# Performance work log

Measured on AMD Instinct MI355X. Metric: run time of the kernel, lower is better.

The kernel has to match this reference:

```python
import jax, jax.numpy as jnp
import numpy as np

D_IN = 512
D_OUT = 512


def setup_inputs() -> dict:
    key = jax.random.key(0)
    ks = jax.random.split(key, 7)
    B, S = 4, 4096
    sc = 1.0 / np.sqrt(D_IN)
    return {
        "x": jax.random.normal(ks[0], (B, S, D_IN), dtype=jnp.float32),
        "Wq": jax.random.normal(ks[1], (D_IN, D_OUT), dtype=jnp.float32) * sc,
        "bq": jnp.zeros((D_OUT,), dtype=jnp.float32),
        "Wk": jax.random.normal(ks[2], (D_IN, D_OUT), dtype=jnp.float32) * sc,
        "bk": jnp.zeros((D_OUT,), dtype=jnp.float32),
        "Wv": jax.random.normal(ks[3], (D_IN, D_OUT), dtype=jnp.float32) * sc,
        "bv": jnp.zeros((D_OUT,), dtype=jnp.float32),
    }


def reference(x, Wq, bq, Wk, bk, Wv, bv):
    # Linear projections
    Q = x @ Wq + bq  # [B,S,Do]
    K = x @ Wk + bk
    V = x @ Wv + bv
    # NOTE: original torch code computes `len(K) ** 1 / 2` which is
    # (len(K)**1)/2 = batch_size / 2 due to operator precedence (not sqrt).
    scale = x.shape[0] / 2.0
    scores = jnp.einsum("bsd,btd->bst", Q, K) / scale  # [B,S,S]
    a = jax.nn.softmax(scores, axis=-1)
    Z = jnp.einsum("bst,btd->bsd", a, V)  # [B,S,Do]
    return Z
```

## Files before the change

### kernel.cpp

```cpp
#include <hip/hip_runtime.h>

typedef _Float16 h8 __attribute__((ext_vector_type(8)));
typedef float f4 __attribute__((ext_vector_type(4)));

#define MFMA16(a, b, c) __builtin_amdgcn_mfma_f32_16x16x32_f16((a), (b), (c), 0, 0, 0)

__device__ static inline void gl_lds16(const void* g, void* l) {
  __builtin_amdgcn_global_load_lds((const __attribute__((address_space(1))) unsigned int*)g,
                                   (__attribute__((address_space(3))) unsigned int*)l, 16, 0, 0);
}

__device__ static inline unsigned encf(float f) {
  unsigned u = __float_as_uint(f);
  return (u & 0x80000000u) ? ~u : (u | 0x80000000u);
}
__device__ static inline float decf(unsigned u) {
  return __uint_as_float((u & 0x80000000u) ? (u ^ 0x80000000u) : ~u);
}


__global__ void wconv_kernel(const float* __restrict__ Wq, const float* __restrict__ Wk,
                             const float* __restrict__ Wv, _Float16* __restrict__ Wt,
                             unsigned* __restrict__ mEnc) {
  int idx = blockIdx.x * 256 + threadIdx.x;
  if (idx < 16384) mEnc[idx] = 0u;
  int z = idx >> 15, rem = idx & 32767;
  int n = rem >> 6, k0 = (rem & 63) << 3;
  const float* W = (z == 0) ? Wq : (z == 1) ? Wk : Wv;
  float sc = (z == 0) ? 0.5f : 1.0f;
  h8 v;
#pragma unroll
  for (int j = 0; j < 8; ++j) v[j] = (_Float16)(W[(k0 + j) * 512 + n] * sc);
  size_t blk = (size_t)((z * 4 + (n >> 7)) * 8 + (k0 >> 6));
  int off = (n & 127) * 64 + ((((k0 >> 3) & 7) ^ (n & 7)) << 3);
  *(h8*)&Wt[blk * 8192 + off] = v;
}

__global__ __launch_bounds__(256, 3)
void proj_kernel(const float* __restrict__ x, const _Float16* __restrict__ Wt,
                 const float* __restrict__ bq, const float* __restrict__ bk,
                 const float* __restrict__ bv,
                 char* __restrict__ Qimg, char* __restrict__ Kimg, char* __restrict__ VTimg) {
  __shared__ _Float16 sMem[16384];
  _Float16* sA = sMem;
  _Float16* sB = sMem + 8192;
  const int tid = threadIdx.x;
  const int wave = tid >> 6, lane = tid & 63;
  const int quad = lane >> 4, lr = lane & 15;
  const int mbase = blockIdx.x * 128, nbase = blockIdx.y * 128, z = blockIdx.z;
  const int sr = tid >> 1, sseg = tid & 1;
  const int rbase = (wave & 1) * 64, cbase = (wave >> 1) * 64;
  const char* WtB = (const char*)Wt + ((size_t)(z * 4 + (nbase >> 7)) * 8) * 16384;

  float4 ax[8];
  f4 acc[4][4];
#pragma unroll
  for (int i = 0; i < 4; ++i)
#pragma unroll
    for (int j = 0; j < 4; ++j) { f4 zz = {0.f, 0.f, 0.f, 0.f}; acc[i][j] = zz; }

  {
    const float4* asrc = (const float4*)&x[(size_t)(mbase + sr) * 512 + sseg * 32];
#pragma unroll
    for (int i = 0; i < 8; ++i) ax[i] = asrc[i];
#pragma unroll
    for (int j = 0; j < 4; ++j)
      gl_lds16(WtB + tid * 16 + j * 4096, (char*)sB + tid * 16 + j * 4096);
  }

  for (int kt = 0; kt < 8; ++kt) {
    if (kt > 0) __syncthreads();
#pragma unroll
    for (int i = 0; i < 4; ++i) {
      h8 v;
      float4 f0 = ax[2 * i], f1 = ax[2 * i + 1];
      v[0] = (_Float16)f0.x; v[1] = (_Float16)f0.y; v[2] = (_Float16)f0.z; v[3] = (_Float16)f0.w;
      v[4] = (_Float16)f1.x; v[5] = (_Float16)f1.y; v[6] = (_Float16)f1.z; v[7] = (_Float16)f1.w;
      *(h8*)&sA[sr * 64 + (((sseg * 4 + i) ^ (sr & 7)) << 3)] = v;
    }
    if (kt > 0) {
#pragma unroll
      for (int j = 0; j < 4; ++j)
        gl_lds16(WtB + kt * 16384 + tid * 16 + j * 4096, (char*)sB + tid * 16 + j * 4096);
    }
    __syncthreads();
    if (kt < 7) {
      const float4* asrc = (const float4*)&x[(size_t)(mbase + sr) * 512 + (kt + 1) * 64 + sseg * 32];
#pragma unroll
      for (int i = 0; i < 8; ++i) ax[i] = asrc[i];
    }
#pragma unroll
    for (int ks = 0; ks < 2; ++ks) {
      h8 a[4], bb[4];
#pragma unroll
      for (int rt = 0; rt < 4; ++rt) {
        const int r = rbase + rt * 16 + lr;
        a[rt] = *(const h8*)&sA[r * 64 + ((((ks << 2) | quad) ^ (lr & 7)) << 3)];
      }
#pragma unroll
      for (int ct = 0; ct < 4; ++ct) {
        const int r = cbase + ct * 16 + lr;
        bb[ct] = *(const h8*)&sB[r * 64 + ((((ks << 2) | quad) ^ (lr & 7)) << 3)];
      }
#pragma unroll
      for (int rt = 0; rt < 4; ++rt)
#pragma unroll
        for (int ct = 0; ct < 4; ++ct)
          acc[rt][ct] = MFMA16(a[rt], bb[ct], acc[rt][ct]);
    }
  }

  const float* bias = (z == 0) ? bq : (z == 1) ? bk : bv;
  const float bscale = (z == 0) ? 0.5f : 1.0f;
  _Float16* sC = sMem;
  __syncthreads();
#pragma unroll
  for (int ct = 0; ct < 4; ++ct) {
    const int dl = cbase + ct * 16 + lr;
    const float bb = bias[nbase + dl] * bscale;
#pragma unroll
    for (int rt = 0; rt < 4; ++rt) {
#pragma unroll
      for (int r = 0; r < 4; ++r) {
        const int sl = rbase + rt * 16 + quad * 4 + r;
        const _Float16 val = (_Float16)(acc[rt][ct][r] + bb);
        if (z == 2) {
          sC[((sl >> 6) << 13) + dl * 64 + ((((sl >> 3) & 7) ^ (dl & 7)) << 3) + (sl & 7)] = val;
        } else {
          sC[((dl >> 6) << 13) + sl * 64 + ((((dl >> 3) & 7) ^ (sl & 7)) << 3) + (dl & 7)] = val;
        }
      }
    }
  }
  __syncthreads();
  const int b_ = mbase >> 12;
  char* dst;
  if (z != 2) {
    char* img = (z == 0) ? Qimg : Kimg;
    dst = img + ((size_t)((b_ * 32 + ((mbase & 4095) >> 7)) * 8 + (nbase >> 6) + (tid >> 7))) * 16384;
  } else {
    dst = VTimg + ((size_t)((b_ * 4 + (nbase >> 7)) * 64 + ((mbase & 4095) >> 6) + (tid >> 7))) * 16384;
  }
  dst += (size_t)(tid & 127) * 128;
#pragma unroll
  for (int k = 0; k < 8; ++k)
    *(int4*)(dst + k * 16) = *(const int4*)&sC[tid * 64 + k * 8];
}

__global__ __launch_bounds__(256, 3)
void qk_kernel(const char* __restrict__ Qimg, const char* __restrict__ Kimg,
               char* __restrict__ S, unsigned* __restrict__ mEnc, int b0, int s0) {
  __shared__ _Float16 sMem[16384];
  _Float16* sA = sMem;
  _Float16* sB = sMem + 8192;
  const int tid = threadIdx.x;
  const int wave = tid >> 6, lane = tid & 63;
  const int quad = lane >> 4, lr = lane & 15;
  const int cb = blockIdx.x;
  const int rbL = blockIdx.z * gridDim.y + blockIdx.y;
  const int b = b0 + blockIdx.z;
  const int rbase = (wave & 1) * 64, cbase = (wave >> 1) * 64;
  const char* Ab = Qimg + ((size_t)((b * 32 + (s0 >> 7) + blockIdx.y) * 8)) * 16384;
  const char* Bb = Kimg + ((size_t)((b * 32 + cb) * 8)) * 16384;

  f4 acc[4][4];
#pragma unroll
  for (int i = 0; i < 4; ++i)
#pragma unroll
    for (int j = 0; j < 4; ++j) { f4 zz = {0.f, 0.f, 0.f, 0.f}; acc[i][j] = zz; }

#pragma unroll
  for (int j = 0; j < 4; ++j) {
    gl_lds16(Ab + tid * 16 + j * 4096, (char*)sA + tid * 16 + j * 4096);
    gl_lds16(Bb + tid * 16 + j * 4096, (char*)sB + tid * 16 + j * 4096);
  }

  for (int kt = 0; kt < 8; ++kt) {
    asm volatile("s_waitcnt vmcnt(0)" ::: "memory");
    __builtin_amdgcn_s_barrier();
    __builtin_amdgcn_sched_barrier(0);
    h8 a[4][2], bb[4][2];
#pragma unroll
    for (int ks = 0; ks < 2; ++ks) {
#pragma unroll
      for (int rt = 0; rt < 4; ++rt) {
        const int r = rbase + rt * 16 + lr;
        a[rt][ks] = *(const h8*)&sA[r * 64 + ((((ks << 2) | quad) ^ (lr & 7)) << 3)];
      }
#pragma unroll
      for (int ct = 0; ct < 4; ++ct) {
        const int r = cbase + ct * 16 + lr;
        bb[ct][ks] = *(const h8*)&sB[r * 64 + ((((ks << 2) | quad) ^ (lr & 7)) << 3)];
      }
    }
    asm volatile("s_waitcnt lgkmcnt(0)" ::: "memory");
    __builtin_amdgcn_s_barrier();
    __builtin_amdgcn_sched_barrier(0);
    if (kt < 7) {
#pragma unroll
      for (int j = 0; j < 4; ++j) {
        gl_lds16(Ab + (kt + 1) * 16384 + tid * 16 + j * 4096, (char*)sA + tid * 16 + j * 4096);
        gl_lds16(Bb + (kt + 1) * 16384 + tid * 16 + j * 4096, (char*)sB + tid * 16 + j * 4096);
      }
    }
    __builtin_amdgcn_s_setprio(1);
#pragma unroll
    for (int ks = 0; ks < 2; ++ks)
#pragma unroll
      for (int rt = 0; rt < 4; ++rt)
#pragma unroll
        for (int ct = 0; ct < 4; ++ct)
          acc[rt][ct] = MFMA16(a[rt][ks], bb[ct][ks], acc[rt][ct]);
    __builtin_amdgcn_s_setprio(0);
  }

  {
    const int growb = b * 4096 + s0 + blockIdx.y * 128;
#pragma unroll
    for (int rt = 0; rt < 4; ++rt) {
#pragma unroll
      for (int r = 0; r < 4; ++r) {
        float mx = fmaxf(fmaxf(acc[rt][0][r], acc[rt][1][r]),
                         fmaxf(acc[rt][2][r], acc[rt][3][r]));
        mx = fmaxf(mx, __shfl_xor(mx, 1));
        mx = fmaxf(mx, __shfl_xor(mx, 2));
        mx = fmaxf(mx, __shfl_xor(mx, 4));
        mx = fmaxf(mx, __shfl_xor(mx, 8));
        if (lr == 0)
          atomicMax(&mEnc[growb + rbase + rt * 16 + quad * 4 + r], encf(mx));
      }
    }
  }

  _Float16* sC = sMem;
  __syncthreads();
#pragma unroll
  for (int ct = 0; ct < 4; ++ct) {
    const int tl = cbase + ct * 16 + lr;
#pragma unroll
    for (int rt = 0; rt < 4; ++rt) {
#pragma unroll
      for (int r = 0; r < 4; ++r) {
        const int sl = rbase + rt * 16 + quad * 4 + r;
        sC[((tl >> 6) << 13) + sl * 64 + ((((tl >> 3) & 7) ^ (sl & 7)) << 3) + (tl & 7)] =
            (_Float16)acc[rt][ct][r];
      }
    }
  }
  __syncthreads();
  char* dst = S + ((size_t)(rbL * 64 + cb * 2 + (tid >> 7))) * 16384 + (size_t)(tid & 127) * 128;
#pragma unroll
  for (int k = 0; k < 8; ++k)
    *(int4*)(dst + k * 16) = *(const int4*)&sC[tid * 64 + k * 8];
}

__global__ __launch_bounds__(256, 4)
void pv_kernel(const char* __restrict__ S, const char* __restrict__ VTimg,
               const unsigned* __restrict__ mEnc, float* __restrict__ out, int b0, int s0) {
  __shared__ _Float16 sMem[12288];
  __shared__ float ls[64];
  _Float16* sA = sMem;
  _Float16* sB = sMem + 4096;
  const int tid = threadIdx.x;
  const int wave = tid >> 6, lane = tid & 63;
  const int quad = lane >> 4, lr = lane & 15;
  const int db = blockIdx.x;
  const int sbL = blockIdx.z * gridDim.y + blockIdx.y;
  const int b = b0 + blockIdx.z;
  const int rbase = (wave & 1) * 32, cbase = (wave >> 1) * 64;
  const char* Ab = S + ((size_t)((sbL >> 1) * 64)) * 16384 + (size_t)(sbL & 1) * 8192;
  const char* Bb = VTimg + ((size_t)((b * 4 + db) * 64)) * 16384;

  const int lrow = tid >> 3;
  const int growb = b * 4096 + s0 + blockIdx.y * 64;
  const float m0 = decf(mEnc[growb + lrow]);
  const float m1 = decf(mEnc[growb + 32 + lrow]);
  float rs0 = 0.f, rs1 = 0.f;

  f4 acc[2][4];
#pragma unroll
  for (int i = 0; i < 2; ++i)
#pragma unroll
    for (int j = 0; j < 4; ++j) { f4 zz = {0.f, 0.f, 0.f, 0.f}; acc[i][j] = zz; }

  {
#pragma unroll
    for (int j = 0; j < 4; ++j)
      gl_lds16(Bb + tid * 16 + j * 4096, (char*)sB + tid * 16 + j * 4096);
    {
      h8 ha = *(const h8*)(Ab + tid * 16);
      h8 w;
#pragma unroll
      for (int u = 0; u < 8; ++u) { float e = __expf((float)ha[u] - m0); w[u] = (_Float16)e; rs0 += e; }
      *(h8*)((char*)sA + tid * 16) = w;
    }
    {
      h8 ha = *(const h8*)(Ab + tid * 16 + 4096);
      h8 w;
#pragma unroll
      for (int u = 0; u < 8; ++u) { float e = __expf((float)ha[u] - m1); w[u] = (_Float16)e; rs1 += e; }
      *(h8*)((char*)sA + tid * 16 + 4096) = w;
    }
  }

  for (int kt = 0; kt < 64; ++kt) {
    asm volatile("s_waitcnt vmcnt(0) lgkmcnt(0)" ::: "memory");
    __builtin_amdgcn_s_barrier();
    __builtin_amdgcn_sched_barrier(0);
    h8 a[2][2], bb[4][2];
#pragma unroll
    for (int ks = 0; ks < 2; ++ks) {
#pragma unroll
      for (int rt = 0; rt < 2; ++rt) {
        const int r = rbase + rt * 16 + lr;
        a[rt][ks] = *(const h8*)&sA[r * 64 + ((((ks << 2) | quad) ^ (lr & 7)) << 3)];
      }
#pragma unroll
      for (int ct = 0; ct < 4; ++ct) {
        const int r = cbase + ct * 16 + lr;
        bb[ct][ks] = *(const h8*)&sB[r * 64 + ((((ks << 2) | quad) ^ (lr & 7)) << 3)];
      }
    }
    h8 ha0, ha1;
    if (kt < 63) {
      ha0 = *(const h8*)(Ab + (kt + 1) * 16384 + tid * 16);
      ha1 = *(const h8*)(Ab + (kt + 1) * 16384 + tid * 16 + 4096);
    }
    asm volatile("s_waitcnt lgkmcnt(0)" ::: "memory");
    __builtin_amdgcn_s_barrier();
    __builtin_amdgcn_sched_barrier(0);
    if (kt < 63) {
#pragma unroll
      for (int j = 0; j < 4; ++j)
        gl_lds16(Bb + (kt + 1) * 16384 + tid * 16 + j * 4096, (char*)sB + tid * 16 + j * 4096);
      h8 w0, w1;
#pragma unroll
      for (int u = 0; u < 8; ++u) { float e = __expf((float)ha0[u] - m0); w0[u] = (_Float16)e; rs0 += e; }
#pragma unroll
      for (int u = 0; u < 8; ++u) { float e = __expf((float)ha1[u] - m1); w1[u] = (_Float16)e; rs1 += e; }
      *(h8*)((char*)sA + tid * 16) = w0;
      *(h8*)((char*)sA + tid * 16 + 4096) = w1;
    }
    __builtin_amdgcn_s_setprio(1);
#pragma unroll
    for (int ks = 0; ks < 2; ++ks)
#pragma unroll
      for (int rt = 0; rt < 2; ++rt)
#pragma unroll
        for (int ct = 0; ct < 4; ++ct)
          acc[rt][ct] = MFMA16(a[rt][ks], bb[ct][ks], acc[rt][ct]);
    __builtin_amdgcn_s_setprio(0);
  }

  rs0 += __shfl_xor(rs0, 1); rs0 += __shfl_xor(rs0, 2); rs0 += __shfl_xor(rs0, 4);
  rs1 += __shfl_xor(rs1, 1); rs1 += __shfl_xor(rs1, 2); rs1 += __shfl_xor(rs1, 4);
  if ((tid & 7) == 0) { ls[lrow] = rs0; ls[32 + lrow] = rs1; }
  __syncthreads();

#pragma unroll
  for (int rt = 0; rt < 2; ++rt) {
#pragma unroll
    for (int r = 0; r < 4; ++r) {
      const int lrw = rbase + rt * 16 + quad * 4 + r;
      const int srow = s0 + blockIdx.y * 64 + lrw;
      const float li = 1.0f / ls[lrw];
      float* op = &out[((size_t)b * 4096 + srow) * 512 + db * 128];
#pragma unroll
      for (int ct = 0; ct < 4; ++ct)
        op[cbase + ct * 16 + lr] = acc[rt][ct][r] * li;
    }
  }
}

extern "C" void kernel_launch(void* const* d_in, const int* in_sizes, int n_in,
                              void* d_out, int out_size, void* d_ws, size_t ws_size,
                              hipStream_t stream) {
  (void)in_sizes; (void)n_in; (void)out_size;
  const float* x  = (const float*)d_in[0];
  const float* Wq = (const float*)d_in[1];
  const float* bq = (const float*)d_in[2];
  const float* Wk = (const float*)d_in[3];
  const float* bk = (const float*)d_in[4];
  const float* Wv = (const float*)d_in[5];
  const float* bv = (const float*)d_in[6];
  float* out = (float*)d_out;
  char* ws = (char*)d_ws;
  char* Qimg  = ws;
  char* Kimg  = ws + ((size_t)16 << 20);
  char* VTimg = ws + ((size_t)32 << 20);
  _Float16* Wt = (_Float16*)(ws + ((size_t)48 << 20));
  unsigned* mEnc = (unsigned*)(ws + ((size_t)50 << 20) - 65536);
  char* Simg   = ws + ((size_t)50 << 20);

  wconv_kernel<<<dim3(384), dim3(256), 0, stream>>>(Wq, Wk, Wv, Wt, mEnc);
  proj_kernel<<<dim3(128, 4, 3), dim3(256), 0, stream>>>(x, Wt, bq, bk, bv, Qimg, Kimg, VTimg);

  const size_t avail = ws_size > ((size_t)50 << 20) ? ws_size - ((size_t)50 << 20) : 0;
  int nchunk, nb, Ms;
  if      (avail >= ((size_t)128 << 20)) { nchunk = 1;  nb = 4; Ms = 4096; }
  else if (avail >= ((size_t)64  << 20)) { nchunk = 2;  nb = 2; Ms = 4096; }
  else if (avail >= ((size_t)32  << 20)) { nchunk = 4;  nb = 1; Ms = 4096; }
  else if (avail >= ((size_t)16  << 20)) { nchunk = 8;  nb = 1; Ms = 2048; }
  else if (avail >= ((size_t)8   << 20)) { nchunk = 16; nb = 1; Ms = 1024; }
  else                                   { nchunk = 32; nb = 1; Ms = 512;  }
  const int chunksPerBatch = 4096 / Ms;

  for (int c = 0; c < nchunk; ++c) {
    int b0, s0;
    if (nb > 1 || Ms == 4096) { b0 = c * nb; s0 = 0; }
    else { b0 = c / chunksPerBatch; s0 = (c % chunksPerBatch) * Ms; }
    qk_kernel<<<dim3(32, Ms / 128, nb), dim3(256), 0, stream>>>(Qimg, Kimg, Simg, mEnc, b0, s0);
    pv_kernel<<<dim3(4, Ms / 64, nb), dim3(256), 0, stream>>>(Simg, VTimg, mEnc, out, b0, s0);
  }
}
```

Before: 405.1 us.

## Widen PV kernel to full 512-column tiles with double-buffered LDS pipeline

The PV kernel now uses 512-thread blocks where each block computes all 512 output columns for 64 rows. Previously four blocks each took a 128-column slice and each recomputed exp over the same S tile. The S tile and the V^T tiles are double-buffered in about 144KB of LDS, so the next tile's global loads overlap the current MFMAs. This leaves one barrier per K step instead of two, and a swizzled block index spreads batches across CUs. The aims are to remove the fourfold redundant exp and S reads and to hide load latency. The cost is one block per CU from the large LDS footprint, more accumulator registers, and a grid four times smaller.

```diff
diff --git a/kernel.cpp b/kernel.cpp
--- a/kernel.cpp
+++ b/kernel.cpp
@@ -254,107 +254,119 @@
     *(int4*)(dst + k * 16) = *(const int4*)&sC[tid * 64 + k * 8];
 }
 
-__global__ __launch_bounds__(256, 4)
+__global__ __launch_bounds__(512, 2)
 void pv_kernel(const char* __restrict__ S, const char* __restrict__ VTimg,
-               const unsigned* __restrict__ mEnc, float* __restrict__ out, int b0, int s0) {
-  __shared__ _Float16 sMem[12288];
+               const unsigned* __restrict__ mEnc, float* __restrict__ out,
+               int b0, int s0, int nyb, int nb) {
+  __shared__ _Float16 sMem[73728];
   __shared__ float ls[64];
-  _Float16* sA = sMem;
-  _Float16* sB = sMem + 4096;
   const int tid = threadIdx.x;
   const int wave = tid >> 6, lane = tid & 63;
   const int quad = lane >> 4, lr = lane & 15;
-  const int db = blockIdx.x;
-  const int sbL = blockIdx.z * gridDim.y + blockIdx.y;
-  const int b = b0 + blockIdx.z;
-  const int rbase = (wave & 1) * 32, cbase = (wave >> 1) * 64;
+  const int flat = blockIdx.x;
+  int bL, yl;
+  if (nb == 4) { bL = (flat & 7) >> 1; yl = ((flat >> 3) << 1) | (flat & 1); }
+  else { bL = flat / nyb; yl = flat - bL * nyb; }
+  const int b = b0 + bL;
+  const int sbL = bL * nyb + yl;
+  const int rbase = (wave & 1) * 32, cbase = (wave >> 1) * 128;
   const char* Ab = S + ((size_t)((sbL >> 1) * 64)) * 16384 + (size_t)(sbL & 1) * 8192;
-  const char* Bb = VTimg + ((size_t)((b * 4 + db) * 64)) * 16384;
+  const char* Bb = VTimg + ((size_t)(b * 4) * 64) * 16384;
 
   const int lrow = tid >> 3;
-  const int growb = b * 4096 + s0 + blockIdx.y * 64;
+  const int growb = b * 4096 + s0 + yl * 64;
   const float m0 = decf(mEnc[growb + lrow]);
-  const float m1 = decf(mEnc[growb + 32 + lrow]);
-  float rs0 = 0.f, rs1 = 0.f;
-
-  f4 acc[2][4];
+  float rs = 0.f;
+
+  f4 acc[2][8];
 #pragma unroll
   for (int i = 0; i < 2; ++i)
 #pragma unroll
-    for (int j = 0; j < 4; ++j) { f4 zz = {0.f, 0.f, 0.f, 0.f}; acc[i][j] = zz; }
+    for (int j = 0; j < 8; ++j) { f4 zz = {0.f, 0.f, 0.f, 0.f}; acc[i][j] = zz; }
 
   {
-#pragma unroll
-    for (int j = 0; j < 4; ++j)
-      gl_lds16(Bb + tid * 16 + j * 4096, (char*)sB + tid * 16 + j * 4096);
-    {
-      h8 ha = *(const h8*)(Ab + tid * 16);
-      h8 w;
-#pragma unroll
-      for (int u = 0; u < 8; ++u) { float e = __expf((float)ha[u] - m0); w[u] = (_Float16)e; rs0 += e; }
-      *(h8*)((char*)sA + tid * 16) = w;
-    }
-    {
-      h8 ha = *(const h8*)(Ab + tid * 16 + 4096);
-      h8 w;
-#pragma unroll
-      for (int u = 0; u < 8; ++u) { float e = __expf((float)ha[u] - m1); w[u] = (_Float16)e; rs1 += e; }
-      *(h8*)((char*)sA + tid * 16 + 4096) = w;
-    }
-  }
-
-  for (int kt = 0; kt < 64; ++kt) {
+    h8 ha = *(const h8*)(Ab + tid * 16);
+#pragma unroll
+    for (int j = 0; j < 8; ++j)
+      gl_lds16(Bb + (size_t)(j >> 1) * 1048576 + (j & 1) * 8192 + tid * 16,
+               (char*)sMem + 16384 + j * 8192 + tid * 16);
+    h8 w;
+#pragma unroll
+    for (int u = 0; u < 8; ++u) { float e = __expf((float)ha[u] - m0); w[u] = (_Float16)e; rs += e; }
+    *(h8*)((char*)sMem + tid * 16) = w;
     asm volatile("s_waitcnt vmcnt(0) lgkmcnt(0)" ::: "memory");
     __builtin_amdgcn_s_barrier();
     __builtin_amdgcn_sched_barrier(0);
-    h8 a[2][2], bb[4][2];
-#pragma unroll
-    for (int ks = 0; ks < 2; ++ks) {
+  }
+
+  for (int kt = 0; kt < 64; ++kt) {
+    const int cur = kt & 1;
+    _Float16* sA = sMem + cur * 4096;
+    _Float16* sB = sMem + 8192 + cur * 32768;
+    char* sAn = (char*)sMem + (cur ^ 1) * 8192;
+    char* sBn = (char*)sMem + 16384 + (cur ^ 1) * 65536;
+    const bool more = (kt < 63);
+    h8 han;
+    if (more) {
+      han = *(const h8*)(Ab + (kt + 1) * 16384 + tid * 16);
+#pragma unroll
+      for (int j = 0; j < 8; ++j)
+        gl_lds16(Bb + (size_t)(j >> 1) * 1048576 + (size_t)(kt + 1) * 16384 + (j & 1) * 8192 + tid * 16,
+                 sBn + j * 8192 + tid * 16);
+    }
+    {
+      h8 a[2], bbf[8];
 #pragma unroll
       for (int rt = 0; rt < 2; ++rt) {
         const int r = rbase + rt * 16 + lr;
-        a[rt][ks] = *(const h8*)&sA[r * 64 + ((((ks << 2) | quad) ^ (lr & 7)) << 3)];
-      }
-#pragma unroll
-      for (int ct = 0; ct < 4; ++ct) {
-        const int r = cbase + ct * 16 + lr;
-        bb[ct][ks] = *(const h8*)&sB[r * 64 + ((((ks << 2) | quad) ^ (lr & 7)) << 3)];
-      }
-    }
-    h8 ha0, ha1;
-    if (kt < 63) {
-      ha0 = *(const h8*)(Ab + (kt + 1) * 16384 + tid * 16);
-      ha1 = *(const h8*)(Ab + (kt + 1) * 16384 + tid * 16 + 4096);
-    }
-    asm volatile("s_waitcnt lgkmcnt(0)" ::: "memory");
+        a[rt] = *(const h8*)&sA[r * 64 + (((quad) ^ (lr & 7)) << 3)];
+      }
+#pragma unroll
+      for (int ct = 0; ct < 8; ++ct) {
+        const int d = cbase + ct * 16 + lr;
+        bbf[ct] = *(const h8*)&sB[d * 64 + (((quad) ^ (lr & 7)) << 3)];
+      }
+      __builtin_amdgcn_s_setprio(1);
+#pragma unroll
+      for (int rt = 0; rt < 2; ++rt)
+#pragma unroll
+        for (int ct = 0; ct < 8; ++ct)
+          acc[rt][ct] = MFMA16(a[rt], bbf[ct], acc[rt][ct]);
+      __builtin_amdgcn_s_setprio(0);
+    }
+    if (more) {
+      h8 w;
+#pragma unroll
+      for (int u = 0; u < 8; ++u) { float e = __expf((float)han[u] - m0); w[u] = (_Float16)e; rs += e; }
+      *(h8*)(sAn + tid * 16) = w;
+    }
+    {
+      h8 a[2], bbf[8];
+#pragma unroll
+      for (int rt = 0; rt < 2; ++rt) {
+        const int r = rbase + rt * 16 + lr;
+        a[rt] = *(const h8*)&sA[r * 64 + (((4 | quad) ^ (lr & 7)) << 3)];
+      }
+#pragma unroll
+      for (int ct = 0; ct < 8; ++ct) {
+        const int d = cbase + ct * 16 + lr;
+        bbf[ct] = *(const h8*)&sB[d * 64 + (((4 | quad) ^ (lr & 7)) << 3)];
+      }
+      __builtin_amdgcn_s_setprio(1);
+#pragma unroll
+      for (int rt = 0; rt < 2; ++rt)
+#pragma unroll
+        for (int ct = 0; ct < 8; ++ct)
+          acc[rt][ct] = MFMA16(a[rt], bbf[ct], acc[rt][ct]);
+      __builtin_amdgcn_s_setprio(0);
+    }
+    asm volatile("s_waitcnt vmcnt(0) lgkmcnt(0)" ::: "memory");
     __builtin_amdgcn_s_barrier();
     __builtin_amdgcn_sched_barrier(0);
-    if (kt < 63) {
-#pragma unroll
-      for (int j = 0; j < 4; ++j)
-        gl_lds16(Bb + (kt + 1) * 16384 + tid * 16 + j * 4096, (char*)sB + tid * 16 + j * 4096);
-      h8 w0, w1;
-#pragma unroll
-      for (int u = 0; u < 8; ++u) { float e = __expf((float)ha0[u] - m0); w0[u] = (_Float16)e; rs0 += e; }
-#pragma unroll
-      for (int u = 0; u < 8; ++u) { float e = __expf((float)ha1[u] - m1); w1[u] = (_Float16)e; rs1 += e; }
-      *(h8*)((char*)sA + tid * 16) = w0;
-      *(h8*)((char*)sA + tid * 16 + 4096) = w1;
-    }
-    __builtin_amdgcn_s_setprio(1);
-#pragma unroll
-    for (int ks = 0; ks < 2; ++ks)
-#pragma unroll
-      for (int rt = 0; rt < 2; ++rt)
-#pragma unroll
-        for (int ct = 0; ct < 4; ++ct)
-          acc[rt][ct] = MFMA16(a[rt][ks], bb[ct][ks], acc[rt][ct]);
-    __builtin_amdgcn_s_setprio(0);
-  }
-
-  rs0 += __shfl_xor(rs0, 1); rs0 += __shfl_xor(rs0, 2); rs0 += __shfl_xor(rs0, 4);
-  rs1 += __shfl_xor(rs1, 1); rs1 += __shfl_xor(rs1, 2); rs1 += __shfl_xor(rs1, 4);
-  if ((tid & 7) == 0) { ls[lrow] = rs0; ls[32 + lrow] = rs1; }
+  }
+
+  rs += __shfl_xor(rs, 1); rs += __shfl_xor(rs, 2); rs += __shfl_xor(rs, 4);
+  if ((tid & 7) == 0) ls[lrow] = rs;
   __syncthreads();
 
 #pragma unroll
@@ -362,11 +374,11 @@
 #pragma unroll
     for (int r = 0; r < 4; ++r) {
       const int lrw = rbase + rt * 16 + quad * 4 + r;
-      const int srow = s0 + blockIdx.y * 64 + lrw;
+      const int srow = s0 + yl * 64 + lrw;
       const float li = 1.0f / ls[lrw];
-      float* op = &out[((size_t)b * 4096 + srow) * 512 + db * 128];
-#pragma unroll
-      for (int ct = 0; ct < 4; ++ct)
+      float* op = &out[((size_t)b * 4096 + srow) * 512];
+#pragma unroll
+      for (int ct = 0; ct < 8; ++ct)
         op[cbase + ct * 16 + lr] = acc[rt][ct][r] * li;
     }
   }
@@ -404,12 +416,13 @@
   else if (avail >= ((size_t)8   << 20)) { nchunk = 16; nb = 1; Ms = 1024; }
   else                                   { nchunk = 32; nb = 1; Ms = 512;  }
   const int chunksPerBatch = 4096 / Ms;
+  const int nyb = Ms / 64;
 
   for (int c = 0; c < nchunk; ++c) {
     int b0, s0;
     if (nb > 1 || Ms == 4096) { b0 = c * nb; s0 = 0; }
     else { b0 = c / chunksPerBatch; s0 = (c % chunksPerBatch) * Ms; }
     qk_kernel<<<dim3(32, Ms / 128, nb), dim3(256), 0, stream>>>(Qimg, Kimg, Simg, mEnc, b0, s0);
-    pv_kernel<<<dim3(4, Ms / 64, nb), dim3(256), 0, stream>>>(Simg, VTimg, mEnc, out, b0, s0);
-  }
-}
+    pv_kernel<<<dim3(nb * nyb), dim3(512), 0, stream>>>(Simg, VTimg, mEnc, out, b0, s0, nyb, nb);
+  }
+}
```

After: 377.0 us. 1.07x faster.
